# Performance work log

Measured on AMD Instinct MI355X. Metric: run time of the kernel, lower is better.

## Reference

```python
import jax, jax.numpy as jnp
import numpy as np
import math

NUM_HEADS = 12
EMBED_DIM = 768

def setup_inputs() -> dict:
    key = jax.random.key(0)
    ks = jax.random.split(key, 9)
    B, T, D = 2, 2048, EMBED_DIM
    s = 1.0 / math.sqrt(D)
    inp = {
        "x": jax.random.normal(ks[0], (B, T, D), dtype=jnp.float32),
        "Wq": jax.random.normal(ks[1], (D, D), dtype=jnp.float32) * s,
        "bq": jnp.zeros((D,), dtype=jnp.float32),
        "Wk": jax.random.normal(ks[2], (D, D), dtype=jnp.float32) * s,
        "bk": jnp.zeros((D,), dtype=jnp.float32),
        "Wv": jax.random.normal(ks[3], (D, D), dtype=jnp.float32) * s,
        "bv": jnp.zeros((D,), dtype=jnp.float32),
        "Wo": jax.random.normal(ks[4], (D, D), dtype=jnp.float32) * s,
        "bo": jnp.zeros((D,), dtype=jnp.float32),
    }
    return inp

def reference(x, Wq, bq, Wk, bk, Wv, bv, Wo, bo):
    B, T, D = x.shape
    H = NUM_HEADS
    Dh = D // H
    # QKV projections, split heads: [B, H, T, Dh]
    def proj(W, b):
        y = x @ W.T + b
        return y.reshape(B, T, H, Dh).transpose(0, 2, 1, 3)
    q = proj(Wq, bq)
    k = proj(Wk, bk)
    v = proj(Wv, bv)
    scores = jnp.einsum('bhtd,bhsd->bhts', q, k) / math.sqrt(Dh)  # [B,H,T,T]
    attn = jax.nn.softmax(scores, axis=-1)
    ctx = jnp.einsum('bhts,bhsd->bhtd', attn, v)  # [B,H,T,Dh]
    ctx = ctx.transpose(0, 2, 1, 3).reshape(B, T, D)
    out = ctx @ Wo.T + bo
    return out
```

## Files before the change

### kernel.cpp

```cpp
#include <hip/hip_runtime.h>
#include <math.h>

using f32x4   = __attribute__((ext_vector_type(4))) float;
using bf16x8  = __attribute__((ext_vector_type(8))) short;

constexpr int Bb = 2;
constexpr int T  = 2048;
constexpr int D  = 768;
constexpr int H  = 12;
constexpr int Dh = 64;
constexpr int M  = Bb * T;
constexpr int NQKV = 3 * D;
#define SCALE_Q 0.18033688011112042f

__device__ __forceinline__ unsigned short f2bf(float f) {
    unsigned u = __float_as_uint(f);
    u += 0x7fffu + ((u >> 16) & 1u);
    return (unsigned short)(u >> 16);
}

__device__ __forceinline__ ushort4 f2bf4(float4 f) {
    return make_ushort4(f2bf(f.x), f2bf(f.y), f2bf(f.z), f2bf(f.w));
}

__device__ __forceinline__ unsigned permpk(float hi_f, float lo_f) {
    return __builtin_amdgcn_perm(__float_as_uint(hi_f), __float_as_uint(lo_f),
                                 0x07060302u);
}

__device__ __forceinline__ void async_copy16(const void* g, void* lds_base) {
    __builtin_amdgcn_global_load_lds(
        (const __attribute__((address_space(1))) unsigned int*)g,
        (__attribute__((address_space(3))) unsigned int*)lds_base, 16, 0, 0);
}

__global__ __launch_bounds__(256) void prep_kernel(
    const float4* __restrict__ x,
    const float4* __restrict__ Wq, const float4* __restrict__ Wk,
    const float4* __restrict__ Wv, const float4* __restrict__ Wo,
    const float* __restrict__ bq, const float* __restrict__ bk, const float* __restrict__ bv,
    ushort4* __restrict__ Xb, ushort4* __restrict__ Wqkvb, ushort4* __restrict__ Wob,
    float* __restrict__ biasS)
{
    const int stride = gridDim.x * 256;
    const int i0 = blockIdx.x * 256 + threadIdx.x;
    const int NX = M * D / 4;
    const int NW = D * D / 4;
    for (int i = i0; i < NX; i += stride) Xb[i] = f2bf4(x[i]);
    for (int i = i0; i < NW; i += stride) {
        Wqkvb[i]          = f2bf4(Wq[i]);
        Wqkvb[NW + i]     = f2bf4(Wk[i]);
        Wqkvb[2 * NW + i] = f2bf4(Wv[i]);
        Wob[i]            = f2bf4(Wo[i]);
    }
    for (int i = i0; i < D; i += stride) {
        biasS[i]         = bq[i];
        biasS[D + i]     = bk[i];
        biasS[2 * D + i] = bv[i];
    }
}

template <int MODE, int TM, int DB>
__global__ __launch_bounds__(256) void gemm_bt_kernel(
    const unsigned short* __restrict__ A, const unsigned short* __restrict__ Bm,
    const float* __restrict__ bias, const int Kdim, const int Ndim,
    float* __restrict__ Cout,
    unsigned short* __restrict__ Qo, unsigned short* __restrict__ Ko,
    unsigned short* __restrict__ Vo)
{
    constexpr int IW  = TM / 32;
    constexpr int NCH = (TM + 128) / 8;
    constexpr int TB  = (TM + 128) * 128;
    __shared__ unsigned short Sm[(TM + 128) * 64 * (DB ? 2 : 1)];
    const int tid  = threadIdx.x;
    const int lane = tid & 63, wv = tid >> 6;
    const int l15  = lane & 15, l4 = lane >> 4;
    const int wr   = wv >> 1,  wc = wv & 1;

    const int lin = blockIdx.y * gridDim.x + blockIdx.x;
    const int gx  = (lin >> 3) % gridDim.x;
    const int gy  = (lin / (8 * gridDim.x)) * 8 + (lin & 7);
    const int row0 = gy * TM, col0 = gx * 128;

    auto stage = [&](int k0, int b) {
        #pragma unroll
        for (int ch0 = 0; ch0 < NCH; ch0 += 4) {
            const int ch = ch0 + wv;
            const int offb = ch * 1024;
            const int off  = offb + lane * 16;
            const int r  = off >> 7;
            const int bl = (off & 127) >> 4;
            const int gc = (bl ^ (r & 7)) << 3;
            const unsigned short* src = (r < TM)
                ? A  + (size_t)(row0 + r) * Kdim + k0 + gc
                : Bm + (size_t)(col0 + (r - TM)) * Kdim + k0 + gc;
            async_copy16(src, (char*)Sm + b * TB + offb);
        }
    };

    f32x4 acc[IW][4];
    #pragma unroll
    for (int i = 0; i < IW; ++i)
        #pragma unroll
        for (int j = 0; j < 4; ++j)
            acc[i][j] = (f32x4){0.f, 0.f, 0.f, 0.f};

    if (DB) stage(0, 0);

    for (int k0 = 0, it = 0; k0 < Kdim; k0 += 64, ++it) {
        const int cur = DB ? (it & 1) : 0;
        __syncthreads();
        if (DB) {
            if (k0 + 64 < Kdim) stage(k0 + 64, cur ^ 1);
        } else {
            stage(k0, 0);
            __syncthreads();
        }
        const char* Sb_ = (const char*)Sm + cur * TB;

        #pragma unroll
        for (int c = 0; c < 2; ++c) {
            bf16x8 af[IW], bfr[4];
            #pragma unroll
            for (int i = 0; i < IW; ++i) {
                const int row = wr * (TM / 2) + i * 16 + l15;
                af[i] = *(const bf16x8*)(Sb_ +
                        row * 128 + (((c << 2) + l4) ^ (row & 7)) * 16);
            }
            #pragma unroll
            for (int j = 0; j < 4; ++j) {
                const int row = TM + wc * 64 + j * 16 + l15;
                bfr[j] = *(const bf16x8*)(Sb_ +
                        row * 128 + (((c << 2) + l4) ^ (row & 7)) * 16);
            }
            #pragma unroll
            for (int i = 0; i < IW; ++i)
                #pragma unroll
                for (int j = 0; j < 4; ++j)
                    acc[i][j] = __builtin_amdgcn_mfma_f32_16x16x32_bf16(af[i], bfr[j], acc[i][j], 0, 0, 0);
        }
    }

    if (MODE == 0) {
        #pragma unroll
        for (int j = 0; j < 4; ++j) {
            const int n = col0 + wc * 64 + j * 16 + l15;
            const float bv_ = bias[n];
            #pragma unroll
            for (int i = 0; i < IW; ++i) {
                #pragma unroll
                for (int r = 0; r < 4; ++r) {
                    const int m = row0 + wr * (TM / 2) + i * 16 + l4 * 4 + r;
                    Cout[(size_t)m * Ndim + n] = acc[i][j][r] + bv_;
                }
            }
        }
    } else {
        #pragma unroll
        for (int j = 0; j < 4; ++j) {
            const int n = col0 + wc * 64 + j * 16 + l15;
            const int which = n / D;
            const int hd = n % D;
            const int h = hd >> 6, d = hd & 63;
            const float bv_ = bias[n];
            if (which == 2) {
                #pragma unroll
                for (int i = 0; i < IW; ++i) {
                    const int m0 = row0 + wr * (TM / 2) + i * 16 + l4 * 4;
                    const int b = m0 >> 11, t = m0 & (T - 1);
                    const int g = (t >> 2) & 3, h16 = (t >> 4) & 1;
                    const int tp = (t & ~31) | (g << 3) | (h16 << 2);
                    float4 v4;
                    v4.x = acc[i][j][0] + bv_; v4.y = acc[i][j][1] + bv_;
                    v4.z = acc[i][j][2] + bv_; v4.w = acc[i][j][3] + bv_;
                    *(ushort4*)&Vo[((size_t)(b * H + h) * Dh + d) * T + tp] = f2bf4(v4);
                }
            } else {
                const float scale = (which == 0) ? SCALE_Q : 1.0f;
                unsigned short* dst = (which == 0) ? Qo : Ko;
                #pragma unroll
                for (int i = 0; i < IW; ++i) {
                    #pragma unroll
                    for (int r = 0; r < 4; ++r) {
                        const int m = row0 + wr * (TM / 2) + i * 16 + l4 * 4 + r;
                        const int b = m >> 11, t = m & (T - 1);
                        dst[((size_t)(b * H + h) * T + t) * Dh + d] =
                            f2bf((acc[i][j][r] + bv_) * scale);
                    }
                }
            }
        }
    }
}

__global__ __launch_bounds__(256) void attn_kernel(
    const unsigned short* __restrict__ Q, const unsigned short* __restrict__ Kg,
    const unsigned short* __restrict__ Vt, unsigned short* __restrict__ Ctx)
{
    __shared__ unsigned short Ks[2][64 * 64];
    __shared__ unsigned short Vs[2][64 * 64];
    const int bh = blockIdx.y;
    const int q0 = blockIdx.x * 64;
    const int tid = threadIdx.x, lane = tid & 63, wv = tid >> 6;
    const int l15 = lane & 15, l4 = lane >> 4;
    const unsigned short* Qp = Q  + (size_t)bh * T * Dh;
    const unsigned short* Kp = Kg + (size_t)bh * T * Dh;
    const unsigned short* Vp = Vt + (size_t)bh * Dh * T;

    bf16x8 qf[2];
    #pragma unroll
    for (int c = 0; c < 2; ++c)
        qf[c] = *(const bf16x8*)&Qp[(size_t)(q0 + wv * 16 + l15) * Dh + c * 32 + l4 * 8];

    const short oneb = (short)0x3F80;
    const bf16x8 onesf = {oneb, oneb, oneb, oneb, oneb, oneb, oneb, oneb};

    auto load_tiles = [&](int kt, int buf) {
        #pragma unroll
        for (int i = 0; i < 2; ++i) {
            const int offb = wv * 2048 + i * 1024;
            const int off  = offb + lane * 16;
            const int r = off >> 7;
            const int blk = (off & 127) >> 4;
            const int gc = (blk ^ (r & 7)) << 3;
            async_copy16(Kp + (size_t)(kt + r) * Dh + gc, (char*)&Ks[buf][0] + offb);
            async_copy16(Vp + (size_t)r * T + kt + gc,    (char*)&Vs[buf][0] + offb);
        }
    };

    load_tiles(0, 0);
    f32x4 o[4], oL;
    #pragma unroll
    for (int nj = 0; nj < 4; ++nj) o[nj] = (f32x4){0.f, 0.f, 0.f, 0.f};
    oL = (f32x4){0.f, 0.f, 0.f, 0.f};

    for (int kt64 = 0; kt64 < T / 64; ++kt64) {
        const int cur = kt64 & 1;
        __syncthreads();
        if (kt64 + 1 < T / 64) load_tiles((kt64 + 1) * 64, cur ^ 1);

        const char* Kb = (const char*)&Ks[cur][0];
        const char* Vb = (const char*)&Vs[cur][0];

        f32x4 Sa[2] = {(f32x4){0.f,0.f,0.f,0.f}, (f32x4){0.f,0.f,0.f,0.f}};
        #pragma unroll
        for (int c = 0; c < 2; ++c) {
            #pragma unroll
            for (int t = 0; t < 2; ++t) {
                const int row = t * 16 + l15;
                bf16x8 kb = *(const bf16x8*)(Kb + row * 128 + (((c << 2) + l4) ^ (row & 7)) * 16);
                Sa[t] = __builtin_amdgcn_mfma_f32_16x16x32_bf16(kb, qf[c], Sa[t], 0, 0, 0);
            }
        }
        #pragma unroll
        for (int t = 0; t < 2; ++t)
            #pragma unroll
            for (int r = 0; r < 4; ++r)
                Sa[t][r] = __builtin_amdgcn_exp2f(Sa[t][r]);
        union { unsigned u[4]; bf16x8 v; } p0;
        p0.u[0] = permpk(Sa[0][1], Sa[0][0]);
        p0.u[1] = permpk(Sa[0][3], Sa[0][2]);
        p0.u[2] = permpk(Sa[1][1], Sa[1][0]);
        p0.u[3] = permpk(Sa[1][3], Sa[1][2]);

        f32x4 Sb[2] = {(f32x4){0.f,0.f,0.f,0.f}, (f32x4){0.f,0.f,0.f,0.f}};
        #pragma unroll
        for (int c = 0; c < 2; ++c) {
            #pragma unroll
            for (int t = 0; t < 2; ++t) {
                const int row = (t + 2) * 16 + l15;
                bf16x8 kb = *(const bf16x8*)(Kb + row * 128 + (((c << 2) + l4) ^ (row & 7)) * 16);
                Sb[t] = __builtin_amdgcn_mfma_f32_16x16x32_bf16(kb, qf[c], Sb[t], 0, 0, 0);
            }
        }

        oL = __builtin_amdgcn_mfma_f32_16x16x32_bf16(p0.v, onesf, oL, 0, 0, 0);
        #pragma unroll
        for (int nj = 0; nj < 4; ++nj) {
            const int row = nj * 16 + l15;
            bf16x8 vb = *(const bf16x8*)(Vb + row * 128 + ((l4) ^ (row & 7)) * 16);
            o[nj] = __builtin_amdgcn_mfma_f32_16x16x32_bf16(p0.v, vb, o[nj], 0, 0, 0);
        }

        #pragma unroll
        for (int t = 0; t < 2; ++t)
            #pragma unroll
            for (int r = 0; r < 4; ++r)
                Sb[t][r] = __builtin_amdgcn_exp2f(Sb[t][r]);
        union { unsigned u[4]; bf16x8 v; } p1;
        p1.u[0] = permpk(Sb[0][1], Sb[0][0]);
        p1.u[1] = permpk(Sb[0][3], Sb[0][2]);
        p1.u[2] = permpk(Sb[1][1], Sb[1][0]);
        p1.u[3] = permpk(Sb[1][3], Sb[1][2]);

        oL = __builtin_amdgcn_mfma_f32_16x16x32_bf16(p1.v, onesf, oL, 0, 0, 0);
        #pragma unroll
        for (int nj = 0; nj < 4; ++nj) {
            const int row = nj * 16 + l15;
            bf16x8 vb = *(const bf16x8*)(Vb + row * 128 + ((4 + l4) ^ (row & 7)) * 16);
            o[nj] = __builtin_amdgcn_mfma_f32_16x16x32_bf16(p1.v, vb, o[nj], 0, 0, 0);
        }
    }

    const int b = bh / H, h = bh % H;
    #pragma unroll
    for (int r = 0; r < 4; ++r) {
        const float inv = 1.0f / oL[r];
        const int t = q0 + wv * 16 + l4 * 4 + r;
        #pragma unroll
        for (int nj = 0; nj < 4; ++nj) {
            const int col = h * 64 + nj * 16 + l15;
            Ctx[(size_t)(b * T + t) * D + col] = f2bf(o[nj][r] * inv);
        }
    }
}

extern "C" void kernel_launch(void* const* d_in, const int* in_sizes, int n_in,
                              void* d_out, int out_size, void* d_ws, size_t ws_size,
                              hipStream_t stream) {
    const float* x  = (const float*)d_in[0];
    const float* Wq = (const float*)d_in[1];
    const float* bq = (const float*)d_in[2];
    const float* Wk = (const float*)d_in[3];
    const float* bk = (const float*)d_in[4];
    const float* Wv = (const float*)d_in[5];
    const float* bv = (const float*)d_in[6];
    const float* Wo = (const float*)d_in[7];
    const float* bo = (const float*)d_in[8];
    float* out = (float*)d_out;

    char* w = (char*)d_ws;
    auto alloc = [&](size_t bytes) {
        char* p = w; w += (bytes + 255) & ~(size_t)255; return p;
    };
    unsigned short* Xb    = (unsigned short*)alloc((size_t)M * D * 2);
    unsigned short* Wqkvb = (unsigned short*)alloc((size_t)NQKV * D * 2);
    unsigned short* Wob   = (unsigned short*)alloc((size_t)D * D * 2);
    float*          biasS = (float*)alloc((size_t)NQKV * 4);
    unsigned short* Qb    = (unsigned short*)alloc((size_t)M * D * 2);
    unsigned short* Kb    = (unsigned short*)alloc((size_t)M * D * 2);
    unsigned short* Vtb   = (unsigned short*)alloc((size_t)M * D * 2);
    unsigned short* Ctxb  = (unsigned short*)alloc((size_t)M * D * 2);

    prep_kernel<<<1024, 256, 0, stream>>>(
        (const float4*)x, (const float4*)Wq, (const float4*)Wk, (const float4*)Wv,
        (const float4*)Wo, bq, bk, bv,
        (ushort4*)Xb, (ushort4*)Wqkvb, (ushort4*)Wob, biasS);

    gemm_bt_kernel<1, 128, 0><<<dim3(NQKV / 128, M / 128), 256, 0, stream>>>(
        Xb, Wqkvb, biasS, D, NQKV, nullptr, Qb, Kb, Vtb);

    attn_kernel<<<dim3(T / 64, Bb * H), 256, 0, stream>>>(Qb, Kb, Vtb, Ctxb);

    gemm_bt_kernel<0, 32, 1><<<dim3(D / 128, M / 32), 256, 0, stream>>>(
        Ctxb, Wob, bo, D, D, out, nullptr, nullptr, nullptr);
}
```

Measured before the change: 156.3 us.

## Split attention key range into two halves and combine partial outputs

The attention kernel now gets a third grid dimension that splits the key/value sequence in two, so each block processes half the keys. Each block writes unnormalized fp32 partial outputs and row sums to workspace. A new combine kernel adds the two halves, normalizes, and writes the bf16 context. The aim is more parallel blocks and shorter per-block loops, at the cost of extra fp32 global-memory traffic and one more kernel launch.

```diff
diff --git a/kernel.cpp b/kernel.cpp
--- a/kernel.cpp
+++ b/kernel.cpp
@@ -11,6 +11,7 @@
 constexpr int Dh = 64;
 constexpr int M  = Bb * T;
 constexpr int NQKV = 3 * D;
+constexpr int NBH = Bb * H;
 #define SCALE_Q 0.18033688011112042f
 
 __device__ __forceinline__ unsigned short f2bf(float f) {
@@ -195,11 +196,13 @@
 
 __global__ __launch_bounds__(256) void attn_kernel(
     const unsigned short* __restrict__ Q, const unsigned short* __restrict__ Kg,
-    const unsigned short* __restrict__ Vt, unsigned short* __restrict__ Ctx)
+    const unsigned short* __restrict__ Vt,
+    float* __restrict__ Po, float* __restrict__ PoL)
 {
     __shared__ unsigned short Ks[2][64 * 64];
     __shared__ unsigned short Vs[2][64 * 64];
     const int bh = blockIdx.y;
+    const int half = blockIdx.z;
     const int q0 = blockIdx.x * 64;
     const int tid = threadIdx.x, lane = tid & 63, wv = tid >> 6;
     const int l15 = lane & 15, l4 = lane >> 4;
@@ -228,16 +231,19 @@
         }
     };
 
-    load_tiles(0, 0);
+    const int NT = T / 128;
+    const int kt0 = half * NT;
+    load_tiles(kt0 * 64, 0);
     f32x4 o[4], oL;
     #pragma unroll
     for (int nj = 0; nj < 4; ++nj) o[nj] = (f32x4){0.f, 0.f, 0.f, 0.f};
     oL = (f32x4){0.f, 0.f, 0.f, 0.f};
 
-    for (int kt64 = 0; kt64 < T / 64; ++kt64) {
-        const int cur = kt64 & 1;
+    for (int it = 0; it < NT; ++it) {
+        const int kt64 = kt0 + it;
+        const int cur = it & 1;
         __syncthreads();
-        if (kt64 + 1 < T / 64) load_tiles((kt64 + 1) * 64, cur ^ 1);
+        if (it + 1 < NT) load_tiles((kt64 + 1) * 64, cur ^ 1);
 
         const char* Kb = (const char*)&Ks[cur][0];
         const char* Vb = (const char*)&Vs[cur][0];
@@ -302,17 +308,33 @@
         }
     }
 
-    const int b = bh / H, h = bh % H;
+    const size_t base = (size_t)(half * NBH + bh) * T;
     #pragma unroll
     for (int r = 0; r < 4; ++r) {
-        const float inv = 1.0f / oL[r];
         const int t = q0 + wv * 16 + l4 * 4 + r;
         #pragma unroll
-        for (int nj = 0; nj < 4; ++nj) {
-            const int col = h * 64 + nj * 16 + l15;
-            Ctx[(size_t)(b * T + t) * D + col] = f2bf(o[nj][r] * inv);
-        }
-    }
+        for (int nj = 0; nj < 4; ++nj)
+            Po[(base + t) * 64 + nj * 16 + l15] = o[nj][r];
+        if (l15 == 0) PoL[base + t] = oL[r];
+    }
+}
+
+__global__ __launch_bounds__(256) void combine_kernel(
+    const float4* __restrict__ Po, const float* __restrict__ PoL,
+    unsigned short* __restrict__ Ctx)
+{
+    const int idx = blockIdx.x * 256 + threadIdx.x;
+    const int d4 = idx & 15;
+    const int rem = idx >> 4;
+    const int t = rem & (T - 1), bh = rem >> 11;
+    const float4 a = Po[(size_t)rem * 16 + d4];
+    const float4 c = Po[(size_t)NBH * T * 16 + (size_t)rem * 16 + d4];
+    const float inv = 1.0f / (PoL[rem] + PoL[NBH * T + rem]);
+    const int b = bh / H, h = bh % H;
+    float4 v;
+    v.x = (a.x + c.x) * inv; v.y = (a.y + c.y) * inv;
+    v.z = (a.z + c.z) * inv; v.w = (a.w + c.w) * inv;
+    *(ushort4*)&Ctx[(size_t)(b * T + t) * D + h * 64 + d4 * 4] = f2bf4(v);
 }
 
 extern "C" void kernel_launch(void* const* d_in, const int* in_sizes, int n_in,
@@ -341,6 +363,8 @@
     unsigned short* Kb    = (unsigned short*)alloc((size_t)M * D * 2);
     unsigned short* Vtb   = (unsigned short*)alloc((size_t)M * D * 2);
     unsigned short* Ctxb  = (unsigned short*)alloc((size_t)M * D * 2);
+    float*          Po    = (float*)alloc((size_t)2 * NBH * T * 64 * 4);
+    float*          PoL   = (float*)alloc((size_t)2 * NBH * T * 4);
 
     prep_kernel<<<1024, 256, 0, stream>>>(
         (const float4*)x, (const float4*)Wq, (const float4*)Wk, (const float4*)Wv,
@@ -350,7 +374,10 @@
     gemm_bt_kernel<1, 128, 0><<<dim3(NQKV / 128, M / 128), 256, 0, stream>>>(
         Xb, Wqkvb, biasS, D, NQKV, nullptr, Qb, Kb, Vtb);
 
-    attn_kernel<<<dim3(T / 64, Bb * H), 256, 0, stream>>>(Qb, Kb, Vtb, Ctxb);
+    attn_kernel<<<dim3(T / 64, NBH, 2), 256, 0, stream>>>(Qb, Kb, Vtb, Po, PoL);
+
+    combine_kernel<<<NBH * T * 16 / 256, 256, 0, stream>>>(
+        (const float4*)Po, PoL, Ctxb);
 
     gemm_bt_kernel<0, 32, 1><<<dim3(D / 128, M / 32), 256, 0, stream>>>(
         Ctxb, Wob, bo, D, D, out, nullptr, nullptr, nullptr);
```

New measurement: 166.8 us. 1.07x slower.

## Switch attention kernel to 32x32x16 MFMA tiles with two waves per block

Applied to the files above, without the earlier changes.

Rewrites the attention inner loop to use 32x32x16 bf16 MFMA instead of 16x16x32, so each wave handles 32 query rows and the block shrinks to 128 threads. The V transposed-store permutation in the QKV GEMM epilogue changes to match the new P-fragment layout. The goal is fewer MFMA issues and LDS fragment reads per unit of work. The cost is a larger accumulator register footprint per wave and fewer waves per block, which may reduce latency hiding.

```diff
diff --git a/kernel.cpp b/kernel.cpp
--- a/kernel.cpp
+++ b/kernel.cpp
@@ -2,6 +2,7 @@
 #include <math.h>
 
 using f32x4   = __attribute__((ext_vector_type(4))) float;
+using f32x16  = __attribute__((ext_vector_type(16))) float;
 using bf16x8  = __attribute__((ext_vector_type(8))) short;
 
 constexpr int Bb = 2;
@@ -12,6 +13,8 @@
 constexpr int M  = Bb * T;
 constexpr int NQKV = 3 * D;
 #define SCALE_Q 0.18033688011112042f
+
+#define Z16 (f32x16){0.f,0.f,0.f,0.f,0.f,0.f,0.f,0.f,0.f,0.f,0.f,0.f,0.f,0.f,0.f,0.f}
 
 __device__ __forceinline__ unsigned short f2bf(float f) {
     unsigned u = __float_as_uint(f);
@@ -168,8 +171,7 @@
                 for (int i = 0; i < IW; ++i) {
                     const int m0 = row0 + wr * (TM / 2) + i * 16 + l4 * 4;
                     const int b = m0 >> 11, t = m0 & (T - 1);
-                    const int g = (t >> 2) & 3, h16 = (t >> 4) & 1;
-                    const int tp = (t & ~31) | (g << 3) | (h16 << 2);
+                    const int tp = (t & ~12) | ((t & 4) << 1) | ((t & 8) >> 1);
                     float4 v4;
                     v4.x = acc[i][j][0] + bv_; v4.y = acc[i][j][1] + bv_;
                     v4.z = acc[i][j][2] + bv_; v4.w = acc[i][j][3] + bv_;
@@ -193,7 +195,7 @@
     }
 }
 
-__global__ __launch_bounds__(256) void attn_kernel(
+__global__ __launch_bounds__(128) void attn_kernel(
     const unsigned short* __restrict__ Q, const unsigned short* __restrict__ Kg,
     const unsigned short* __restrict__ Vt, unsigned short* __restrict__ Ctx)
 {
@@ -202,23 +204,23 @@
     const int bh = blockIdx.y;
     const int q0 = blockIdx.x * 64;
     const int tid = threadIdx.x, lane = tid & 63, wv = tid >> 6;
-    const int l15 = lane & 15, l4 = lane >> 4;
+    const int l31 = lane & 31, hs = lane >> 5;
     const unsigned short* Qp = Q  + (size_t)bh * T * Dh;
     const unsigned short* Kp = Kg + (size_t)bh * T * Dh;
     const unsigned short* Vp = Vt + (size_t)bh * Dh * T;
 
-    bf16x8 qf[2];
+    bf16x8 qf[4];
     #pragma unroll
-    for (int c = 0; c < 2; ++c)
-        qf[c] = *(const bf16x8*)&Qp[(size_t)(q0 + wv * 16 + l15) * Dh + c * 32 + l4 * 8];
+    for (int c = 0; c < 4; ++c)
+        qf[c] = *(const bf16x8*)&Qp[(size_t)(q0 + wv * 32 + l31) * Dh + c * 16 + hs * 8];
 
     const short oneb = (short)0x3F80;
     const bf16x8 onesf = {oneb, oneb, oneb, oneb, oneb, oneb, oneb, oneb};
 
     auto load_tiles = [&](int kt, int buf) {
         #pragma unroll
-        for (int i = 0; i < 2; ++i) {
-            const int offb = wv * 2048 + i * 1024;
+        for (int i = 0; i < 4; ++i) {
+            const int offb = wv * 4096 + i * 1024;
             const int off  = offb + lane * 16;
             const int r = off >> 7;
             const int blk = (off & 127) >> 4;
@@ -229,10 +231,8 @@
     };
 
     load_tiles(0, 0);
-    f32x4 o[4], oL;
-    #pragma unroll
-    for (int nj = 0; nj < 4; ++nj) o[nj] = (f32x4){0.f, 0.f, 0.f, 0.f};
-    oL = (f32x4){0.f, 0.f, 0.f, 0.f};
+    f32x16 o[2], oL;
+    o[0] = Z16; o[1] = Z16; oL = Z16;
 
     for (int kt64 = 0; kt64 < T / 64; ++kt64) {
         const int cur = kt64 & 1;
@@ -242,75 +242,71 @@
         const char* Kb = (const char*)&Ks[cur][0];
         const char* Vb = (const char*)&Vs[cur][0];
 
-        f32x4 Sa[2] = {(f32x4){0.f,0.f,0.f,0.f}, (f32x4){0.f,0.f,0.f,0.f}};
-        #pragma unroll
-        for (int c = 0; c < 2; ++c) {
-            #pragma unroll
-            for (int t = 0; t < 2; ++t) {
-                const int row = t * 16 + l15;
-                bf16x8 kb = *(const bf16x8*)(Kb + row * 128 + (((c << 2) + l4) ^ (row & 7)) * 16);
-                Sa[t] = __builtin_amdgcn_mfma_f32_16x16x32_bf16(kb, qf[c], Sa[t], 0, 0, 0);
-            }
-        }
-        #pragma unroll
-        for (int t = 0; t < 2; ++t)
-            #pragma unroll
-            for (int r = 0; r < 4; ++r)
-                Sa[t][r] = __builtin_amdgcn_exp2f(Sa[t][r]);
-        union { unsigned u[4]; bf16x8 v; } p0;
-        p0.u[0] = permpk(Sa[0][1], Sa[0][0]);
-        p0.u[1] = permpk(Sa[0][3], Sa[0][2]);
-        p0.u[2] = permpk(Sa[1][1], Sa[1][0]);
-        p0.u[3] = permpk(Sa[1][3], Sa[1][2]);
-
-        f32x4 Sb[2] = {(f32x4){0.f,0.f,0.f,0.f}, (f32x4){0.f,0.f,0.f,0.f}};
-        #pragma unroll
-        for (int c = 0; c < 2; ++c) {
-            #pragma unroll
-            for (int t = 0; t < 2; ++t) {
-                const int row = (t + 2) * 16 + l15;
-                bf16x8 kb = *(const bf16x8*)(Kb + row * 128 + (((c << 2) + l4) ^ (row & 7)) * 16);
-                Sb[t] = __builtin_amdgcn_mfma_f32_16x16x32_bf16(kb, qf[c], Sb[t], 0, 0, 0);
-            }
-        }
-
-        oL = __builtin_amdgcn_mfma_f32_16x16x32_bf16(p0.v, onesf, oL, 0, 0, 0);
-        #pragma unroll
-        for (int nj = 0; nj < 4; ++nj) {
-            const int row = nj * 16 + l15;
-            bf16x8 vb = *(const bf16x8*)(Vb + row * 128 + ((l4) ^ (row & 7)) * 16);
-            o[nj] = __builtin_amdgcn_mfma_f32_16x16x32_bf16(p0.v, vb, o[nj], 0, 0, 0);
-        }
-
-        #pragma unroll
-        for (int t = 0; t < 2; ++t)
-            #pragma unroll
-            for (int r = 0; r < 4; ++r)
-                Sb[t][r] = __builtin_amdgcn_exp2f(Sb[t][r]);
-        union { unsigned u[4]; bf16x8 v; } p1;
-        p1.u[0] = permpk(Sb[0][1], Sb[0][0]);
-        p1.u[1] = permpk(Sb[0][3], Sb[0][2]);
-        p1.u[2] = permpk(Sb[1][1], Sb[1][0]);
-        p1.u[3] = permpk(Sb[1][3], Sb[1][2]);
-
-        oL = __builtin_amdgcn_mfma_f32_16x16x32_bf16(p1.v, onesf, oL, 0, 0, 0);
-        #pragma unroll
-        for (int nj = 0; nj < 4; ++nj) {
-            const int row = nj * 16 + l15;
-            bf16x8 vb = *(const bf16x8*)(Vb + row * 128 + ((4 + l4) ^ (row & 7)) * 16);
-            o[nj] = __builtin_amdgcn_mfma_f32_16x16x32_bf16(p1.v, vb, o[nj], 0, 0, 0);
+        f32x16 S0 = Z16;
+        #pragma unroll
+        for (int c = 0; c < 4; ++c) {
+            const int row = l31;
+            bf16x8 kb = *(const bf16x8*)(Kb + row * 128 + (((c << 1) + hs) ^ (row & 7)) * 16);
+            S0 = __builtin_amdgcn_mfma_f32_32x32x16_bf16(kb, qf[c], S0, 0, 0, 0);
+        }
+        #pragma unroll
+        for (int r = 0; r < 16; ++r)
+            S0[r] = __builtin_amdgcn_exp2f(S0[r]);
+        union { unsigned u[4]; bf16x8 v; } pa0, pa1;
+        pa0.u[0] = permpk(S0[1],  S0[0]);  pa0.u[1] = permpk(S0[3],  S0[2]);
+        pa0.u[2] = permpk(S0[5],  S0[4]);  pa0.u[3] = permpk(S0[7],  S0[6]);
+        pa1.u[0] = permpk(S0[9],  S0[8]);  pa1.u[1] = permpk(S0[11], S0[10]);
+        pa1.u[2] = permpk(S0[13], S0[12]); pa1.u[3] = permpk(S0[15], S0[14]);
+
+        f32x16 S1 = Z16;
+        #pragma unroll
+        for (int c = 0; c < 4; ++c) {
+            const int row = 32 + l31;
+            bf16x8 kb = *(const bf16x8*)(Kb + row * 128 + (((c << 1) + hs) ^ (row & 7)) * 16);
+            S1 = __builtin_amdgcn_mfma_f32_32x32x16_bf16(kb, qf[c], S1, 0, 0, 0);
+        }
+
+        oL = __builtin_amdgcn_mfma_f32_32x32x16_bf16(pa0.v, onesf, oL, 0, 0, 0);
+        oL = __builtin_amdgcn_mfma_f32_32x32x16_bf16(pa1.v, onesf, oL, 0, 0, 0);
+        #pragma unroll
+        for (int h2 = 0; h2 < 2; ++h2) {
+            const int row = h2 * 32 + l31;
+            bf16x8 v0 = *(const bf16x8*)(Vb + row * 128 + ((0 + hs) ^ (row & 7)) * 16);
+            o[h2] = __builtin_amdgcn_mfma_f32_32x32x16_bf16(pa0.v, v0, o[h2], 0, 0, 0);
+            bf16x8 v1 = *(const bf16x8*)(Vb + row * 128 + ((2 + hs) ^ (row & 7)) * 16);
+            o[h2] = __builtin_amdgcn_mfma_f32_32x32x16_bf16(pa1.v, v1, o[h2], 0, 0, 0);
+        }
+
+        #pragma unroll
+        for (int r = 0; r < 16; ++r)
+            S1[r] = __builtin_amdgcn_exp2f(S1[r]);
+        union { unsigned u[4]; bf16x8 v; } pa2, pa3;
+        pa2.u[0] = permpk(S1[1],  S1[0]);  pa2.u[1] = permpk(S1[3],  S1[2]);
+        pa2.u[2] = permpk(S1[5],  S1[4]);  pa2.u[3] = permpk(S1[7],  S1[6]);
+        pa3.u[0] = permpk(S1[9],  S1[8]);  pa3.u[1] = permpk(S1[11], S1[10]);
+        pa3.u[2] = permpk(S1[13], S1[12]); pa3.u[3] = permpk(S1[15], S1[14]);
+
+        oL = __builtin_amdgcn_mfma_f32_32x32x16_bf16(pa2.v, onesf, oL, 0, 0, 0);
+        oL = __builtin_amdgcn_mfma_f32_32x32x16_bf16(pa3.v, onesf, oL, 0, 0, 0);
+        #pragma unroll
+        for (int h2 = 0; h2 < 2; ++h2) {
+            const int row = h2 * 32 + l31;
+            bf16x8 v2 = *(const bf16x8*)(Vb + row * 128 + ((4 + hs) ^ (row & 7)) * 16);
+            o[h2] = __builtin_amdgcn_mfma_f32_32x32x16_bf16(pa2.v, v2, o[h2], 0, 0, 0);
+            bf16x8 v3 = *(const bf16x8*)(Vb + row * 128 + ((6 + hs) ^ (row & 7)) * 16);
+            o[h2] = __builtin_amdgcn_mfma_f32_32x32x16_bf16(pa3.v, v3, o[h2], 0, 0, 0);
         }
     }
 
     const int b = bh / H, h = bh % H;
     #pragma unroll
-    for (int r = 0; r < 4; ++r) {
-        const float inv = 1.0f / oL[r];
-        const int t = q0 + wv * 16 + l4 * 4 + r;
-        #pragma unroll
-        for (int nj = 0; nj < 4; ++nj) {
-            const int col = h * 64 + nj * 16 + l15;
-            Ctx[(size_t)(b * T + t) * D + col] = f2bf(o[nj][r] * inv);
+    for (int reg = 0; reg < 16; ++reg) {
+        const float inv = 1.0f / oL[reg];
+        const int t = q0 + wv * 32 + (reg & 3) + 8 * (reg >> 2) + 4 * hs;
+        #pragma unroll
+        for (int h2 = 0; h2 < 2; ++h2) {
+            const int col = h * 64 + h2 * 32 + l31;
+            Ctx[(size_t)(b * T + t) * D + col] = f2bf(o[h2][reg] * inv);
         }
     }
 }
@@ -350,7 +346,7 @@
     gemm_bt_kernel<1, 128, 0><<<dim3(NQKV / 128, M / 128), 256, 0, stream>>>(
         Xb, Wqkvb, biasS, D, NQKV, nullptr, Qb, Kb, Vtb);
 
-    attn_kernel<<<dim3(T / 64, Bb * H), 256, 0, stream>>>(Qb, Kb, Vtb, Ctxb);
+    attn_kernel<<<dim3(T / 64, Bb * H), 128, 0, stream>>>(Qb, Kb, Vtb, Ctxb);
 
     gemm_bt_kernel<0, 32, 1><<<dim3(D / 128, M / 32), 256, 0, stream>>>(
         Ctxb, Wob, bo, D, D, out, nullptr, nullptr, nullptr);
```

After: 170.7 us. 1.09x slower.
